# Kernel optimization log

Hardware: AMD Instinct MI355X
Metric: run time of the kernel (lower is better)

## Reference

```python
import jax, jax.numpy as jnp
import numpy as np

LEN_MASK = 2   # hardcoded in the original forward
TOP_POOL = 5   # positions drawn from top-5 intensity slots


def setup_inputs() -> dict:
    key = jax.random.key(0)
    k1, k2 = jax.random.split(key)
    B, S = 16384, 1024
    x = jax.random.randint(k1, (B, S), 0, 10000, dtype=jnp.int64)
    intensity_ = jax.random.uniform(k2, (B, 1, S), dtype=jnp.float32)
    return {"x": x, "intensity_": intensity_, "max_pred": 5}


def reference(x, intensity_, max_pred):
    # x: [B, S] int token ids; intensity_: [B, 1, S] float
    intensity = jnp.squeeze(intensity_, axis=1)            # [B, S]
    B, S = x.shape
    # top-5 positions by descending intensity (== argsort(desc)[:5])
    top5 = jax.lax.top_k(intensity, TOP_POOL)[1]           # [B, 5] int
    # randperm(5)[:2] per sample, vectorized: argsort of iid uniforms
    rkey = jax.random.key(42)
    u = jax.random.uniform(rkey, (B, TOP_POOL))
    sel = jnp.argsort(u, axis=-1)[:, :LEN_MASK]            # [B, 2] random 2-of-5
    mask_pos2 = jnp.take_along_axis(top5, sel, axis=1)     # [B, 2]
    # mask_bool: all False (rand > 1), True at the chosen positions
    mask_bool = jnp.zeros((B, S), dtype=bool).at[
        jnp.arange(B)[:, None], mask_pos2
    ].set(True)                                            # [B, S]
    mask_x = jnp.where(mask_bool, jnp.asarray(1, x.dtype), x)   # masked_fill(x, mask_bool, 1)
    mask_token2 = jnp.take_along_axis(x, mask_pos2, axis=1)     # [B, 2]
    # pad to max_pred with zeros (original branch: len_mask < max_pred)
    n_pad = max_pred - LEN_MASK
    mask_pos = jnp.pad(mask_pos2, ((0, 0), (0, n_pad))).astype(jnp.int64)
    mask_token = jnp.pad(mask_token2, ((0, 0), (0, n_pad))).astype(jnp.int64)
    return mask_x, mask_token, mask_pos
```

## Files before the change

kernel.cpp:

```cpp
#include <hip/hip_runtime.h>
#include <stdint.h>


#define S_LEN 1024
#define TOPK 5

__device__ __forceinline__ uint32_t rotl32(uint32_t x, int r) {
    return (x << r) | (x >> (32 - r));
}

__device__ __forceinline__ void threefry2x32(uint32_t k0, uint32_t k1,
                                             uint32_t x0, uint32_t x1,
                                             uint32_t& o0, uint32_t& o1) {
    uint32_t ks2 = k0 ^ k1 ^ 0x1BD11BDAu;
    x0 += k0; x1 += k1;
#define TF_R4(a,b,c,d) \
    x0 += x1; x1 = rotl32(x1,a); x1 ^= x0; \
    x0 += x1; x1 = rotl32(x1,b); x1 ^= x0; \
    x0 += x1; x1 = rotl32(x1,c); x1 ^= x0; \
    x0 += x1; x1 = rotl32(x1,d); x1 ^= x0;
    TF_R4(13,15,26,6);   x0 += k1;  x1 += ks2 + 1u;
    TF_R4(17,29,16,24);  x0 += ks2; x1 += k0  + 2u;
    TF_R4(13,15,26,6);   x0 += k0;  x1 += k1  + 3u;
    TF_R4(17,29,16,24);  x0 += k1;  x1 += ks2 + 4u;
    TF_R4(13,15,26,6);   x0 += ks2; x1 += k0  + 5u;
#undef TF_R4
    o0 = x0; o1 = x1;
}

__device__ __forceinline__ void cswap32(uint32_t& a, uint32_t& b) {
    const uint32_t hi = max(a, b);
    const uint32_t lo = min(a, b);
    a = hi; b = lo;
}

__device__ __forceinline__ uint64_t u64max(uint64_t a, uint64_t b) {
    return (a > b) ? a : b;
}

__global__ __launch_bounds__(256)
void mask_kernel(const float* __restrict__ inten,
                 const int*   __restrict__ x,
                 int* __restrict__ out_x,
                 int* __restrict__ out_tok,
                 int* __restrict__ out_pos,
                 int B) {
    const int wave = threadIdx.x >> 6;
    const int lane = threadIdx.x & 63;
    const int row  = blockIdx.x * 4 + wave;
    if (row >= B) return;

    const float* irow = inten + (size_t)row * S_LEN;
    const int*   xrow = x     + (size_t)row * S_LEN;

    const float4 v0 = *reinterpret_cast<const float4*>(irow + 0   + lane * 4);
    const float4 v1 = *reinterpret_cast<const float4*>(irow + 256 + lane * 4);
    const float4 v2 = *reinterpret_cast<const float4*>(irow + 512 + lane * 4);
    const float4 v3 = *reinterpret_cast<const float4*>(irow + 768 + lane * 4);
    const int4 xv0 = *reinterpret_cast<const int4*>(xrow + 0   + lane * 4);
    const int4 xv1 = *reinterpret_cast<const int4*>(xrow + 256 + lane * 4);
    const int4 xv2 = *reinterpret_cast<const int4*>(xrow + 512 + lane * 4);
    const int4 xv3 = *reinterpret_cast<const int4*>(xrow + 768 + lane * 4);

    uint32_t t0 = 0, t1 = 0, t2 = 0, t3 = 0, t4 = 0;
#define INS(f, rnk) {                                                   \
        const uint32_t m = (uint32_t)((f) * 8388608.0f);                \
        const uint32_t key = (m << 4) | (uint32_t)(15 - (rnk));        \
        t4 = max(t4, key);                                              \
        cswap32(t3, t4); cswap32(t2, t3); cswap32(t1, t2); cswap32(t0, t1); }
    INS(v0.x, 0)  INS(v0.y, 1)  INS(v0.z, 2)  INS(v0.w, 3)
    INS(v1.x, 4)  INS(v1.y, 5)  INS(v1.z, 6)  INS(v1.w, 7)
    INS(v2.x, 8)  INS(v2.y, 9)  INS(v2.z, 10) INS(v2.w, 11)
    INS(v3.x, 12) INS(v3.y, 13) INS(v3.z, 14) INS(v3.w, 15)
#undef INS

#define TO64(t) ({                                                       \
        const uint32_t r_ = 15u - ((t) & 15u);                           \
        const uint32_t s_ = ((r_ >> 2) << 8) + ((uint32_t)lane << 2) + (r_ & 3u); \
        (((uint64_t)((t) >> 4)) << 10) | (uint64_t)(1023u - s_); })
    uint64_t T0 = TO64(t0), T1 = TO64(t1), T2 = TO64(t2), T3 = TO64(t3), T4 = TO64(t4);
#undef TO64

    int idx0 = 0, idx1 = 0, idx2 = 0, idx3 = 0, idx4 = 0;
#pragma unroll
    for (int r = 0; r < TOPK; ++r) {
        uint64_t w = T0;
#pragma unroll
        for (int off = 1; off < 64; off <<= 1) {
            const uint64_t o =
                (uint64_t)__shfl_xor((unsigned long long)w, off, 64);
            w = u64max(w, o);
        }
        if (T0 == w) { T0 = T1; T1 = T2; T2 = T3; T3 = T4; T4 = 0; }
        const int s = 1023 - (int)((uint32_t)w & 1023u);
        if (r == 0) idx0 = s;
        else if (r == 1) idx1 = s;
        else if (r == 2) idx2 = s;
        else if (r == 3) idx3 = s;
        else idx4 = s;
    }

    uint32_t kj = 0xFFFFFFFFu;
    if (lane < TOPK) {
        const uint32_t g = (uint32_t)row * 5u + (uint32_t)lane;
        uint32_t o0, o1;
        threefry2x32(0u, 42u, 0u, g, o0, o1);
        const uint32_t bits = o0 ^ o1;
        kj = ((bits >> 9) << 3) | (uint32_t)lane;
    }
    const uint32_t q0 = __shfl(kj, 0, 64);
    const uint32_t q1 = __shfl(kj, 1, 64);
    const uint32_t q2 = __shfl(kj, 2, 64);
    const uint32_t q3 = __shfl(kj, 3, 64);
    const uint32_t q4 = __shfl(kj, 4, 64);

    const uint32_t mn1 = min(min(min(q0, q1), min(q2, q3)), q4);
    const int sel0 = (int)(mn1 & 7u);
    const uint32_t e0 = (q0 == mn1) ? 0xFFFFFFFFu : q0;
    const uint32_t e1 = (q1 == mn1) ? 0xFFFFFFFFu : q1;
    const uint32_t e2 = (q2 == mn1) ? 0xFFFFFFFFu : q2;
    const uint32_t e3 = (q3 == mn1) ? 0xFFFFFFFFu : q3;
    const uint32_t e4 = (q4 == mn1) ? 0xFFFFFFFFu : q4;
    const uint32_t mn2 = min(min(min(e0, e1), min(e2, e3)), e4);
    const int sel1 = (int)(mn2 & 7u);

    const int p0 = (sel0 == 0) ? idx0 : (sel0 == 1) ? idx1 : (sel0 == 2) ? idx2
                 : (sel0 == 3) ? idx3 : idx4;
    const int p1 = (sel1 == 0) ? idx0 : (sel1 == 1) ? idx1 : (sel1 == 2) ? idx2
                 : (sel1 == 3) ? idx3 : idx4;

    int* orow = out_x + (size_t)row * S_LEN;
#define STORE4(xv, base) {                                               \
        int4 o = (xv);                                                   \
        const int sb = (base) + lane * 4;                                \
        if (sb + 0 == p0 || sb + 0 == p1) o.x = 1;                       \
        if (sb + 1 == p0 || sb + 1 == p1) o.y = 1;                       \
        if (sb + 2 == p0 || sb + 2 == p1) o.z = 1;                       \
        if (sb + 3 == p0 || sb + 3 == p1) o.w = 1;                       \
        *reinterpret_cast<int4*>(orow + sb) = o; }
    STORE4(xv0, 0)
    STORE4(xv1, 256)
    STORE4(xv2, 512)
    STORE4(xv3, 768)
#undef STORE4

    if (lane == 0) {
        const int xa = xrow[p0];
        const int xb = xrow[p1];
        int* tk = out_tok + (size_t)row * 5;
        tk[0] = xa; tk[1] = xb; tk[2] = 0; tk[3] = 0; tk[4] = 0;
        int* pp = out_pos + (size_t)row * 5;
        pp[0] = p0; pp[1] = p1; pp[2] = 0; pp[3] = 0; pp[4] = 0;
    }
}

extern "C" void kernel_launch(void* const* d_in, const int* in_sizes, int n_in,
                              void* d_out, int out_size, void* d_ws, size_t ws_size,
                              hipStream_t stream) {
    const int*   x     = (const int*)d_in[0];
    const float* inten = (const float*)d_in[1];

    const int BS = in_sizes[0];
    const int B  = BS / S_LEN;

    int* out     = (int*)d_out;
    int* out_tok = out + (size_t)B * S_LEN;
    int* out_pos = out_tok + (size_t)B * TOPK;

    dim3 grid((B + 3) / 4), block(256);
    hipLaunchKernelGGL(mask_kernel, grid, block, 0, stream,
                       inten, x, out, out_tok, out_pos, B);
}
```

Baseline: 174.6 us.

## Stop top-k wave reduction early at needed rank and use 32-bit keys

Replaces the fixed five rounds of 64-bit cross-lane max reductions with a loop that runs only up to the highest rank actually selected by the random draw. Each round now uses a packed 32-bit key, with one index bit dropped and recovered through a ballot and shuffle from the winning lane. It also adds an occupancy hint to launch bounds and a scheduling barrier after the loads. This is meant to cut shuffle and ALU latency per row, which dominates a kernel that is not fully bandwidth bound. The risks are a data-dependent, divergent-free but variable trip count, and a change in how exact ties are broken.

After: 174.8 us. No clear change (+0.1%).

```diff
diff --git a/kernel.cpp b/kernel.cpp
--- a/kernel.cpp
+++ b/kernel.cpp
@@ -34,11 +34,7 @@
     a = hi; b = lo;
 }
 
-__device__ __forceinline__ uint64_t u64max(uint64_t a, uint64_t b) {
-    return (a > b) ? a : b;
-}
-
-__global__ __launch_bounds__(256)
+__global__ __launch_bounds__(256, 8)
 void mask_kernel(const float* __restrict__ inten,
                  const int*   __restrict__ x,
                  int* __restrict__ out_x,
@@ -61,11 +57,12 @@
     const int4 xv1 = *reinterpret_cast<const int4*>(xrow + 256 + lane * 4);
     const int4 xv2 = *reinterpret_cast<const int4*>(xrow + 512 + lane * 4);
     const int4 xv3 = *reinterpret_cast<const int4*>(xrow + 768 + lane * 4);
+    __builtin_amdgcn_sched_barrier(0);
 
     uint32_t t0 = 0, t1 = 0, t2 = 0, t3 = 0, t4 = 0;
 #define INS(f, rnk) {                                                   \
         const uint32_t m = (uint32_t)((f) * 8388608.0f);                \
-        const uint32_t key = (m << 4) | (uint32_t)(15 - (rnk));        \
+        const uint32_t key = (m << 4) | (uint32_t)(15 - (rnk));         \
         t4 = max(t4, key);                                              \
         cswap32(t3, t4); cswap32(t2, t3); cswap32(t1, t2); cswap32(t0, t1); }
     INS(v0.x, 0)  INS(v0.y, 1)  INS(v0.z, 2)  INS(v0.w, 3)
@@ -73,32 +70,6 @@
     INS(v2.x, 8)  INS(v2.y, 9)  INS(v2.z, 10) INS(v2.w, 11)
     INS(v3.x, 12) INS(v3.y, 13) INS(v3.z, 14) INS(v3.w, 15)
 #undef INS
-
-#define TO64(t) ({                                                       \
-        const uint32_t r_ = 15u - ((t) & 15u);                           \
-        const uint32_t s_ = ((r_ >> 2) << 8) + ((uint32_t)lane << 2) + (r_ & 3u); \
-        (((uint64_t)((t) >> 4)) << 10) | (uint64_t)(1023u - s_); })
-    uint64_t T0 = TO64(t0), T1 = TO64(t1), T2 = TO64(t2), T3 = TO64(t3), T4 = TO64(t4);
-#undef TO64
-
-    int idx0 = 0, idx1 = 0, idx2 = 0, idx3 = 0, idx4 = 0;
-#pragma unroll
-    for (int r = 0; r < TOPK; ++r) {
-        uint64_t w = T0;
-#pragma unroll
-        for (int off = 1; off < 64; off <<= 1) {
-            const uint64_t o =
-                (uint64_t)__shfl_xor((unsigned long long)w, off, 64);
-            w = u64max(w, o);
-        }
-        if (T0 == w) { T0 = T1; T1 = T2; T2 = T3; T3 = T4; T4 = 0; }
-        const int s = 1023 - (int)((uint32_t)w & 1023u);
-        if (r == 0) idx0 = s;
-        else if (r == 1) idx1 = s;
-        else if (r == 2) idx2 = s;
-        else if (r == 3) idx3 = s;
-        else idx4 = s;
-    }
 
     uint32_t kj = 0xFFFFFFFFu;
     if (lane < TOPK) {
@@ -124,10 +95,24 @@
     const uint32_t mn2 = min(min(min(e0, e1), min(e2, e3)), e4);
     const int sel1 = (int)(mn2 & 7u);
 
-    const int p0 = (sel0 == 0) ? idx0 : (sel0 == 1) ? idx1 : (sel0 == 2) ? idx2
-                 : (sel0 == 3) ? idx3 : idx4;
-    const int p1 = (sel1 == 0) ? idx0 : (sel1 == 1) ? idx1 : (sel1 == 2) ? idx2
-                 : (sel1 == 3) ? idx3 : idx4;
+    const int nr = (sel0 > sel1 ? sel0 : sel1) + 1;
+
+    int p0 = 0, p1 = 0;
+    for (int r = 0; r < nr; ++r) {
+        const uint32_t rank = 15u - (t0 & 15u);
+        const uint32_t s_h  = ((rank >> 2) << 8) + ((uint32_t)lane << 2) + (rank & 3u);
+        const uint32_t wk   = ((t0 >> 4) << 9) | ((1023u - s_h) >> 1);
+        uint32_t w = wk;
+#pragma unroll
+        for (int off = 1; off < 64; off <<= 1)
+            w = max(w, (uint32_t)__shfl_xor(w, off, 64));
+        const unsigned long long bal = __ballot(wk == w);
+        const int wl  = (int)__ffsll(bal) - 1;
+        const int s_w = __shfl((int)s_h, wl, 64);
+        if (wk == w) { t0 = t1; t1 = t2; t2 = t3; t3 = t4; t4 = 0; }
+        if (r == sel0) p0 = s_w;
+        if (r == sel1) p1 = s_w;
+    }
 
     int* orow = out_x + (size_t)row * S_LEN;
 #define STORE4(xv, base) {                                               \
```
